# Kernel tuning notes

Hardware: AMD Instinct MI355X
Metric: run time of the kernel (lower is better)

## Reference

```python
import jax, jax.numpy as jnp
import numpy as np

D_MODEL = 1024
N_EXPERTS = 8
TOP_K = 2
D_HIDDEN = 4 * D_MODEL


def setup_inputs() -> dict:
    key = jax.random.key(0)
    ks = jax.random.split(key, 6)
    x = jax.random.normal(ks[0], (4, 2048, D_MODEL), dtype=jnp.float32)
    gate_w = jax.random.normal(ks[1], (N_EXPERTS, D_MODEL), dtype=jnp.float32) * 0.02
    w1 = jax.random.normal(ks[2], (N_EXPERTS, D_MODEL, D_HIDDEN), dtype=jnp.float32) * 0.02
    b1 = jnp.zeros((N_EXPERTS, D_HIDDEN), dtype=jnp.float32)
    w2 = jax.random.normal(ks[3], (N_EXPERTS, D_HIDDEN, D_MODEL), dtype=jnp.float32) * 0.02
    b2 = jnp.zeros((N_EXPERTS, D_MODEL), dtype=jnp.float32)
    return {"x": x, "gate_w": gate_w, "w1": w1, "b1": b1, "w2": w2, "b2": b2}


def reference(x, gate_w, w1, b1, w2, b2):
    B, S, D = x.shape
    xf = x.reshape(-1, D)                               # [T, D]
    logits = xf @ gate_w.T                              # [T, E]
    top_vals, top_idx = jax.lax.top_k(logits, TOP_K)    # [T, K]
    rw = jax.nn.softmax(top_vals.astype(jnp.float32), axis=-1).astype(x.dtype)  # [T, K]
    out = jnp.zeros_like(xf)
    for i in range(N_EXPERTS):
        # combined routing weight for expert i per token (0 if not selected)
        cw = jnp.sum(jnp.where(top_idx == i, rw, jnp.zeros_like(rw)), axis=-1)  # [T]
        h = jax.nn.relu(xf @ w1[i] + b1[i])             # [T, 4D]
        y = h @ w2[i] + b2[i]                           # [T, D]
        out = out + y * cw[:, None]
    return out.reshape(B, S, D)
```

## Files before the change

### kernel.cpp

```cpp
#include <hip/hip_runtime.h>
#include <stdint.h>

#define D_MODEL   1024
#define N_EXPERTS 8
#define D_HIDDEN  4096
#define T_TOKENS  8192
#define N_SLOTS   (T_TOKENS * 2)
#define MAX_TILES 136

typedef __bf16 bf16x8 __attribute__((ext_vector_type(8)));
typedef float  f32x4  __attribute__((ext_vector_type(4)));
typedef unsigned short ushort8 __attribute__((ext_vector_type(8)));

__device__ __forceinline__ unsigned short f2bf(float f) {
    unsigned int u = __float_as_uint(f);
    u += 0x7fffu + ((u >> 16) & 1u);
    return (unsigned short)(u >> 16);
}
__device__ __forceinline__ float bf2f(unsigned short v) {
    return __uint_as_float((unsigned int)v << 16);
}

__device__ __forceinline__ void gl_lds16(const void* g, void* l) {
    __builtin_amdgcn_global_load_lds(
        (const __attribute__((address_space(1))) unsigned int*)g,
        (__attribute__((address_space(3))) unsigned int*)l, 16, 0, 0);
}

__global__ __launch_bounds__(256) void gate_kernel(
    const float* __restrict__ x, const float* __restrict__ gw,
    unsigned short* __restrict__ xb,
    int* __restrict__ route_pack, float* __restrict__ route_w,
    int* __restrict__ cnt)
{
    __shared__ float gws[N_EXPERTS * D_MODEL];
    __shared__ int hist[N_EXPERTS];
    int tid = threadIdx.x;
    for (int i = tid * 4; i < N_EXPERTS * D_MODEL; i += 256 * 4)
        *(float4*)&gws[i] = *(const float4*)&gw[i];
    if (tid < N_EXPERTS) hist[tid] = 0;
    __syncthreads();

    int wave = tid >> 6, lane = tid & 63;
    for (int tt = 0; tt < 4; tt++) {
        int t = blockIdx.x * 16 + wave * 4 + tt;
        const float* xr = x + (size_t)t * D_MODEL;

        float acc[N_EXPERTS];
        for (int e = 0; e < N_EXPERTS; e++) acc[e] = 0.f;
        for (int i = 0; i < 4; i++) {
            float4 xv = *(const float4*)&xr[lane * 4 + i * 256];
            ushort4 o;
            o.x = f2bf(xv.x); o.y = f2bf(xv.y); o.z = f2bf(xv.z); o.w = f2bf(xv.w);
            *(ushort4*)&xb[(size_t)t * D_MODEL + lane * 4 + i * 256] = o;
            for (int e = 0; e < N_EXPERTS; e++) {
                float4 gv = *(const float4*)&gws[e * D_MODEL + lane * 4 + i * 256];
                acc[e] += xv.x * gv.x + xv.y * gv.y + xv.z * gv.z + xv.w * gv.w;
            }
        }
        for (int e = 0; e < N_EXPERTS; e++)
            for (int off = 32; off >= 1; off >>= 1)
                acc[e] += __shfl_xor(acc[e], off, 64);

        if (lane == 0) {
            int e0 = 0; float v0 = acc[0];
            for (int e = 1; e < N_EXPERTS; e++) if (acc[e] > v0) { v0 = acc[e]; e0 = e; }
            int e1 = (e0 == 0) ? 1 : 0; float v1 = acc[e1];
            for (int e = 0; e < N_EXPERTS; e++)
                if (e != e0 && acc[e] > v1) { v1 = acc[e]; e1 = e; }
            float w0 = 1.f / (1.f + __expf(v1 - v0));
            route_pack[t] = e0 | (e1 << 8);
            route_w[2 * t]     = w0;
            route_w[2 * t + 1] = 1.f - w0;
            atomicAdd(&hist[e0], 1);
            atomicAdd(&hist[e1], 1);
        }
    }
    __syncthreads();
    if (tid < N_EXPERTS) atomicAdd(&cnt[tid], hist[tid]);
}

__global__ void offsets_kernel(const int* __restrict__ cnt,
                               int* __restrict__ off, int* __restrict__ cnt2)
{
    if (threadIdx.x == 0) {
        int a = 0;
        for (int e = 0; e < N_EXPERTS; e++) { off[e] = a; a += cnt[e]; cnt2[e] = 0; }
        off[N_EXPERTS] = a;
    }
}

__global__ __launch_bounds__(64) void scatter_kernel(
    const int* __restrict__ route_pack, const int* __restrict__ off,
    int* __restrict__ cnt2, int* __restrict__ tok_id, int* __restrict__ inv)
{
    int lane = threadIdx.x;
    int t = blockIdx.x * 64 + lane;
    int p  = route_pack[t];
    int e0 = p & 0xff, e1 = (p >> 8) & 0xff;

    unsigned long long m0[N_EXPERTS], m1[N_EXPERTS];
    for (int e = 0; e < N_EXPERTS; e++) {
        m0[e] = __ballot(e0 == e);
        m1[e] = __ballot(e1 == e);
    }
    int mybase = 0;
    if (lane < N_EXPERTS)
        mybase = atomicAdd(&cnt2[lane], __popcll(m0[lane]) + __popcll(m1[lane]));

    unsigned long long lt = (1ull << lane) - 1ull;
    int b0 = __shfl(mybase, e0);
    int s0 = off[e0] + b0 + (int)__popcll(m0[e0] & lt);
    int b1 = __shfl(mybase, e1);
    int s1 = off[e1] + b1 + (int)__popcll(m0[e1]) + (int)__popcll(m1[e1] & lt);

    tok_id[s0] = t;
    tok_id[s1] = t;
    inv[2 * t]     = s0;
    inv[2 * t + 1] = s1;
}

template <int R, int C>
__global__ __launch_bounds__(256) void transpose_convert_kernel(
    const float* __restrict__ src, unsigned short* __restrict__ dst)
{
    __shared__ float tile[64 * 68];
    int e = blockIdx.z;
    const float* s = src + (size_t)e * R * C;
    unsigned short* d = dst + (size_t)e * R * C;
    int r0 = blockIdx.y * 64, c0 = blockIdx.x * 64;
    int t = threadIdx.x;
    {
        int r = t >> 4, c4 = (t & 15) * 4;
        for (int p = 0; p < 4; p++, r += 16)
            *(float4*)&tile[r * 68 + c4] = *(const float4*)&s[(size_t)(r0 + r) * C + c0 + c4];
    }
    __syncthreads();
    {
        int c = t >> 2, rblk = (t & 3) * 8;
        for (int q = 0; q < 2; q++) {
            int rr = q * 32 + rblk;
            ushort8 o;
            for (int j = 0; j < 8; j++) o[j] = f2bf(tile[(rr + j) * 68 + c]);
            *(ushort8*)&d[(size_t)(c0 + c) * R + r0 + rr] = o;
        }
    }
}

__global__ __launch_bounds__(256) void gemm1_kernel(
    const unsigned short* __restrict__ xb, const unsigned short* __restrict__ w1t,
    const float* __restrict__ b1, const int* __restrict__ tok_id,
    const int* __restrict__ off, unsigned short* __restrict__ h)
{
    __shared__ unsigned short smem[2 * 128 * 64];
    unsigned short* As = smem;
    unsigned short* Bs = smem + 128 * 64;
    unsigned short* stage = smem;

    int bx = blockIdx.x;
    int e = -1, slot0 = 0, end = 0;
    {
        int acc = 0;
        for (int i = 0; i < N_EXPERTS; i++) {
            int s = off[i], en = off[i + 1];
            int nt = (en - s + 127) >> 7;
            if (e < 0 && bx < acc + nt) { e = i; slot0 = s + (bx - acc) * 128; end = en; }
            acc += nt;
        }
        if (e < 0) return;
    }
    int n0 = blockIdx.y * 128;
    int tid = threadIdx.x, wave = tid >> 6, lane = tid & 63;
    int lr = lane >> 3, lc = lane & 7;

    f32x4 acc[4][4];
    const f32x4 zero = {0.f, 0.f, 0.f, 0.f};
    for (int i = 0; i < 4; i++) for (int j = 0; j < 4; j++) acc[i][j] = zero;

    const unsigned short* gA[4];
    const unsigned short* gB[4];
    unsigned short* lA[4];
    unsigned short* lB[4];
#pragma unroll
    for (int c = 0; c < 4; c++) {
        int arow = wave * 32 + c * 8 + lr;
        int slot = min(slot0 + arow, end - 1);
        gA[c] = xb + (size_t)tok_id[slot] * D_MODEL + lc * 8;
        gB[c] = w1t + ((size_t)e * D_HIDDEN + n0 + arow) * D_MODEL + lc * 8;
        lA[c] = &As[(wave * 32 + c * 8) * 64];
        lB[c] = &Bs[(wave * 32 + c * 8) * 64];
    }

    int wm = wave & 1, wn = wave >> 1;
    int row16 = lane & 15, q8 = (lane >> 4) * 8;
    for (int k0 = 0; k0 < D_MODEL; k0 += 64) {
#pragma unroll
        for (int c = 0; c < 4; c++) {
            gl_lds16(gA[c] + k0, lA[c]);
            gl_lds16(gB[c] + k0, lB[c]);
        }
        __syncthreads();
#pragma unroll
        for (int ks = 0; ks < 2; ks++) {
            bf16x8 af[4], bfr[4];
#pragma unroll
            for (int i = 0; i < 4; i++)
                af[i] = *(const bf16x8*)&As[(wm * 64 + i * 16 + row16) * 64 + ks * 32 + q8];
#pragma unroll
            for (int j = 0; j < 4; j++)
                bfr[j] = *(const bf16x8*)&Bs[(wn * 64 + j * 16 + row16) * 64 + ks * 32 + q8];
#pragma unroll
            for (int i = 0; i < 4; i++)
#pragma unroll
                for (int j = 0; j < 4; j++)
                    acc[i][j] = __builtin_amdgcn_mfma_f32_16x16x32_bf16(af[i], bfr[j], acc[i][j], 0, 0, 0);
        }
        __syncthreads();
    }

    int quad = lane >> 4, col16 = lane & 15;
    for (int p = 0; p < 2; p++) {
        __syncthreads();
        if (wm == p) {
            for (int j = 0; j < 4; j++) {
                int n = n0 + wn * 64 + j * 16 + col16;
                float bias = b1[e * D_HIDDEN + n];
                for (int i = 0; i < 4; i++)
                    for (int r = 0; r < 4; r++) {
                        float v = acc[i][j][r] + bias;
                        v = v > 0.f ? v : 0.f;
                        stage[(i * 16 + quad * 4 + r) * 136 + wn * 64 + j * 16 + col16] = f2bf(v);
                    }
            }
        }
        __syncthreads();
        int row = tid >> 4, coff = (tid & 15) * 8;
        for (int rr = row; rr < 64; rr += 16) {
            int slot = slot0 + p * 64 + rr;
            if (slot < end)
                *(ushort8*)&h[(size_t)slot * D_HIDDEN + n0 + coff] =
                    *(const ushort8*)&stage[rr * 136 + coff];
        }
    }
}

__global__ __launch_bounds__(256) void gemm2_kernel(
    const unsigned short* __restrict__ h, const unsigned short* __restrict__ w2t,
    const float* __restrict__ b2, const int* __restrict__ off,
    unsigned short* __restrict__ y)
{
    __shared__ unsigned short smem[2 * 128 * 64];
    unsigned short* As = smem;
    unsigned short* Bs = smem + 128 * 64;
    unsigned short* stage = smem;

    int bx = blockIdx.x;
    int e = -1, slot0 = 0, end = 0;
    {
        int acc = 0;
        for (int i = 0; i < N_EXPERTS; i++) {
            int s = off[i], en = off[i + 1];
            int nt = (en - s + 127) >> 7;
            if (e < 0 && bx < acc + nt) { e = i; slot0 = s + (bx - acc) * 128; end = en; }
            acc += nt;
        }
        if (e < 0) return;
    }
    int n0 = blockIdx.y * 128;
    int tid = threadIdx.x, wave = tid >> 6, lane = tid & 63;
    int lr = lane >> 3, lc = lane & 7;

    f32x4 acc[4][4];
    const f32x4 zero = {0.f, 0.f, 0.f, 0.f};
    for (int i = 0; i < 4; i++) for (int j = 0; j < 4; j++) acc[i][j] = zero;

    const unsigned short* gA[4];
    const unsigned short* gB[4];
    unsigned short* lA[4];
    unsigned short* lB[4];
#pragma unroll
    for (int c = 0; c < 4; c++) {
        int arow = wave * 32 + c * 8 + lr;
        int slot = min(slot0 + arow, end - 1);
        gA[c] = h + (size_t)slot * D_HIDDEN + lc * 8;
        gB[c] = w2t + ((size_t)e * D_MODEL + n0 + arow) * D_HIDDEN + lc * 8;
        lA[c] = &As[(wave * 32 + c * 8) * 64];
        lB[c] = &Bs[(wave * 32 + c * 8) * 64];
    }

    int wm = wave & 1, wn = wave >> 1;
    int row16 = lane & 15, q8 = (lane >> 4) * 8;
    for (int k0 = 0; k0 < D_HIDDEN; k0 += 64) {
#pragma unroll
        for (int c = 0; c < 4; c++) {
            gl_lds16(gA[c] + k0, lA[c]);
            gl_lds16(gB[c] + k0, lB[c]);
        }
        __syncthreads();
#pragma unroll
        for (int ks = 0; ks < 2; ks++) {
            bf16x8 af[4], bfr[4];
#pragma unroll
            for (int i = 0; i < 4; i++)
                af[i] = *(const bf16x8*)&As[(wm * 64 + i * 16 + row16) * 64 + ks * 32 + q8];
#pragma unroll
            for (int j = 0; j < 4; j++)
                bfr[j] = *(const bf16x8*)&Bs[(wn * 64 + j * 16 + row16) * 64 + ks * 32 + q8];
#pragma unroll
            for (int i = 0; i < 4; i++)
#pragma unroll
                for (int j = 0; j < 4; j++)
                    acc[i][j] = __builtin_amdgcn_mfma_f32_16x16x32_bf16(af[i], bfr[j], acc[i][j], 0, 0, 0);
        }
        __syncthreads();
    }

    int quad = lane >> 4, col16 = lane & 15;
    for (int p = 0; p < 2; p++) {
        __syncthreads();
        if (wm == p) {
            for (int j = 0; j < 4; j++) {
                int n = n0 + wn * 64 + j * 16 + col16;
                float bias = b2[e * D_MODEL + n];
                for (int i = 0; i < 4; i++)
                    for (int r = 0; r < 4; r++) {
                        float v = acc[i][j][r] + bias;
                        stage[(i * 16 + quad * 4 + r) * 136 + wn * 64 + j * 16 + col16] = f2bf(v);
                    }
            }
        }
        __syncthreads();
        int row = tid >> 4, coff = (tid & 15) * 8;
        for (int rr = row; rr < 64; rr += 16) {
            int slot = slot0 + p * 64 + rr;
            if (slot < end)
                *(ushort8*)&y[(size_t)slot * D_MODEL + n0 + coff] =
                    *(const ushort8*)&stage[rr * 136 + coff];
        }
    }
}

__global__ __launch_bounds__(256) void combine_kernel(
    const unsigned short* __restrict__ y, const int* __restrict__ inv,
    const float* __restrict__ rw, float* __restrict__ out)
{
    int wave = threadIdx.x >> 6, lane = threadIdx.x & 63;
    int t = blockIdx.x * 4 + wave;
    int s0 = inv[2 * t], s1 = inv[2 * t + 1];
    float w0 = rw[2 * t], w1 = rw[2 * t + 1];
    const unsigned short* y0 = y + (size_t)s0 * D_MODEL;
    const unsigned short* y1 = y + (size_t)s1 * D_MODEL;
    float* orow = out + (size_t)t * D_MODEL;
    int c = lane * 16;
    for (int hh = 0; hh < 2; hh++) {
        ushort8 a = *(const ushort8*)&y0[c + hh * 8];
        ushort8 b = *(const ushort8*)&y1[c + hh * 8];
        float4 o0, o1;
        o0.x = w0 * bf2f(a[0]) + w1 * bf2f(b[0]);
        o0.y = w0 * bf2f(a[1]) + w1 * bf2f(b[1]);
        o0.z = w0 * bf2f(a[2]) + w1 * bf2f(b[2]);
        o0.w = w0 * bf2f(a[3]) + w1 * bf2f(b[3]);
        o1.x = w0 * bf2f(a[4]) + w1 * bf2f(b[4]);
        o1.y = w0 * bf2f(a[5]) + w1 * bf2f(b[5]);
        o1.z = w0 * bf2f(a[6]) + w1 * bf2f(b[6]);
        o1.w = w0 * bf2f(a[7]) + w1 * bf2f(b[7]);
        *(float4*)&orow[c + hh * 8]     = o0;
        *(float4*)&orow[c + hh * 8 + 4] = o1;
    }
}

extern "C" void kernel_launch(void* const* d_in, const int* in_sizes, int n_in,
                              void* d_out, int out_size, void* d_ws, size_t ws_size,
                              hipStream_t stream)
{
    const float* x      = (const float*)d_in[0];
    const float* gate_w = (const float*)d_in[1];
    const float* w1     = (const float*)d_in[2];
    const float* b1     = (const float*)d_in[3];
    const float* w2     = (const float*)d_in[4];
    const float* b2     = (const float*)d_in[5];
    float* out = (float*)d_out;

    char* ws = (char*)d_ws;
    size_t o = 0;
    auto alloc = [&](size_t bytes) { void* p = ws + o; o += (bytes + 255) & ~(size_t)255; return p; };
    int*   cnt        = (int*)alloc(32);
    int*   cnt2       = (int*)alloc(32);
    int*   off        = (int*)alloc(64);
    int*   route_pack = (int*)alloc((size_t)T_TOKENS * 4);
    float* route_w    = (float*)alloc((size_t)T_TOKENS * 8);
    int*   tok_id     = (int*)alloc((size_t)N_SLOTS * 4);
    int*   inv        = (int*)alloc((size_t)T_TOKENS * 8);
    unsigned short* xb  = (unsigned short*)alloc((size_t)T_TOKENS * D_MODEL * 2);
    unsigned short* w1t = (unsigned short*)alloc((size_t)N_EXPERTS * D_MODEL * D_HIDDEN * 2);
    unsigned short* w2t = (unsigned short*)alloc((size_t)N_EXPERTS * D_MODEL * D_HIDDEN * 2);
    unsigned short* h   = (unsigned short*)alloc((size_t)N_SLOTS * D_HIDDEN * 2);
    unsigned short* y   = w1t;

    hipMemsetAsync(cnt, 0, 32, stream);

    gate_kernel<<<T_TOKENS / 16, 256, 0, stream>>>(x, gate_w, xb, route_pack, route_w, cnt);
    offsets_kernel<<<1, 64, 0, stream>>>(cnt, off, cnt2);
    scatter_kernel<<<T_TOKENS / 64, 64, 0, stream>>>(route_pack, off, cnt2, tok_id, inv);
    transpose_convert_kernel<D_MODEL, D_HIDDEN>
        <<<dim3(D_HIDDEN / 64, D_MODEL / 64, N_EXPERTS), dim3(256), 0, stream>>>(w1, w1t);
    transpose_convert_kernel<D_HIDDEN, D_MODEL>
        <<<dim3(D_MODEL / 64, D_HIDDEN / 64, N_EXPERTS), dim3(256), 0, stream>>>(w2, w2t);
    gemm1_kernel<<<dim3(MAX_TILES, D_HIDDEN / 128), 256, 0, stream>>>(xb, w1t, b1, tok_id, off, h);
    gemm2_kernel<<<dim3(MAX_TILES, D_MODEL / 128), 256, 0, stream>>>(h, w2t, b2, off, y);
    combine_kernel<<<T_TOKENS / 4, 256, 0, stream>>>(y, inv, route_w, out);
}
```

Measured before the change: 902.1 us.

## Double-buffer LDS, XOR-swizzle tiles, and remap blocks across XCDs in expert GEMMs

Both expert GEMM kernels now keep two LDS buffers so the next K-slice's global-to-LDS loads are issued while MFMAs run on the current slice, which drops one barrier per iteration. Columns are XOR-swizzled on load and read to avoid LDS bank conflicts. The 2D grid is flattened to 1D and remapped so consecutive tiles of the same row block land on the same XCD, aiming for better L2 reuse of weights and activations. The cost is double the LDS per block (64KB), which may lower occupancy.

```diff
diff --git a/kernel.cpp b/kernel.cpp
--- a/kernel.cpp
+++ b/kernel.cpp
@@ -152,12 +152,16 @@
     const float* __restrict__ b1, const int* __restrict__ tok_id,
     const int* __restrict__ off, unsigned short* __restrict__ h)
 {
-    __shared__ unsigned short smem[2 * 128 * 64];
-    unsigned short* As = smem;
-    unsigned short* Bs = smem + 128 * 64;
+    constexpr int NT = D_HIDDEN / 128;
+    constexpr int BUF = 128 * 64;
+    __shared__ unsigned short smem[2 * 2 * BUF];
     unsigned short* stage = smem;
 
-    int bx = blockIdx.x;
+    int wg = blockIdx.x;
+    int sz = (wg & 7) * ((MAX_TILES * NT) >> 3) + (wg >> 3);
+    int bx = sz >> 5;
+    int n0 = (sz & (NT - 1)) * 128;
+
     int e = -1, slot0 = 0, end = 0;
     {
         int acc = 0;
@@ -169,9 +173,9 @@
         }
         if (e < 0) return;
     }
-    int n0 = blockIdx.y * 128;
     int tid = threadIdx.x, wave = tid >> 6, lane = tid & 63;
     int lr = lane >> 3, lc = lane & 7;
+    int lcs = lc ^ lr;
 
     f32x4 acc[4][4];
     const f32x4 zero = {0.f, 0.f, 0.f, 0.f};
@@ -179,36 +183,50 @@
 
     const unsigned short* gA[4];
     const unsigned short* gB[4];
-    unsigned short* lA[4];
-    unsigned short* lB[4];
+    int ldsA[4], ldsB[4];
 #pragma unroll
     for (int c = 0; c < 4; c++) {
         int arow = wave * 32 + c * 8 + lr;
         int slot = min(slot0 + arow, end - 1);
-        gA[c] = xb + (size_t)tok_id[slot] * D_MODEL + lc * 8;
-        gB[c] = w1t + ((size_t)e * D_HIDDEN + n0 + arow) * D_MODEL + lc * 8;
-        lA[c] = &As[(wave * 32 + c * 8) * 64];
-        lB[c] = &Bs[(wave * 32 + c * 8) * 64];
+        gA[c] = xb + (size_t)tok_id[slot] * D_MODEL + lcs * 8;
+        gB[c] = w1t + ((size_t)e * D_HIDDEN + n0 + arow) * D_MODEL + lcs * 8;
+        ldsA[c] = (wave * 32 + c * 8) * 64;
+        ldsB[c] = BUF + (wave * 32 + c * 8) * 64;
     }
 
     int wm = wave & 1, wn = wave >> 1;
-    int row16 = lane & 15, q8 = (lane >> 4) * 8;
-    for (int k0 = 0; k0 < D_MODEL; k0 += 64) {
-#pragma unroll
-        for (int c = 0; c < 4; c++) {
-            gl_lds16(gA[c] + k0, lA[c]);
-            gl_lds16(gB[c] + k0, lB[c]);
-        }
-        __syncthreads();
+    int row16 = lane & 15, q4 = lane >> 4;
+    int sx = row16 & 7;
+
+#pragma unroll
+    for (int c = 0; c < 4; c++) {
+        gl_lds16(gA[c], smem + ldsA[c]);
+        gl_lds16(gB[c], smem + ldsB[c]);
+    }
+    __syncthreads();
+
+    int cur = 0;
+    for (int t = 0; t < D_MODEL / 64; t++) {
+        if (t + 1 < D_MODEL / 64) {
+            int k0 = (t + 1) * 64;
+            unsigned short* dst = smem + (cur ^ 1) * 2 * BUF;
+#pragma unroll
+            for (int c = 0; c < 4; c++) {
+                gl_lds16(gA[c] + k0, dst + ldsA[c]);
+                gl_lds16(gB[c] + k0, dst + ldsB[c]);
+            }
+        }
+        const unsigned short* As = smem + cur * 2 * BUF;
+        const unsigned short* Bs = As + BUF;
 #pragma unroll
         for (int ks = 0; ks < 2; ks++) {
             bf16x8 af[4], bfr[4];
 #pragma unroll
             for (int i = 0; i < 4; i++)
-                af[i] = *(const bf16x8*)&As[(wm * 64 + i * 16 + row16) * 64 + ks * 32 + q8];
+                af[i] = *(const bf16x8*)&As[(wm * 64 + i * 16 + row16) * 64 + (((ks * 4 + q4) ^ sx) * 8)];
 #pragma unroll
             for (int j = 0; j < 4; j++)
-                bfr[j] = *(const bf16x8*)&Bs[(wn * 64 + j * 16 + row16) * 64 + ks * 32 + q8];
+                bfr[j] = *(const bf16x8*)&Bs[(wn * 64 + j * 16 + row16) * 64 + (((ks * 4 + q4) ^ sx) * 8)];
 #pragma unroll
             for (int i = 0; i < 4; i++)
 #pragma unroll
@@ -216,6 +234,7 @@
                     acc[i][j] = __builtin_amdgcn_mfma_f32_16x16x32_bf16(af[i], bfr[j], acc[i][j], 0, 0, 0);
         }
         __syncthreads();
+        cur ^= 1;
     }
 
     int quad = lane >> 4, col16 = lane & 15;
@@ -249,12 +268,16 @@
     const float* __restrict__ b2, const int* __restrict__ off,
     unsigned short* __restrict__ y)
 {
-    __shared__ unsigned short smem[2 * 128 * 64];
-    unsigned short* As = smem;
-    unsigned short* Bs = smem + 128 * 64;
+    constexpr int NT = D_MODEL / 128;
+    constexpr int BUF = 128 * 64;
+    __shared__ unsigned short smem[2 * 2 * BUF];
     unsigned short* stage = smem;
 
-    int bx = blockIdx.x;
+    int wg = blockIdx.x;
+    int sz = (wg & 7) * ((MAX_TILES * NT) >> 3) + (wg >> 3);
+    int bx = sz >> 3;
+    int n0 = (sz & (NT - 1)) * 128;
+
     int e = -1, slot0 = 0, end = 0;
     {
         int acc = 0;
@@ -266,9 +289,9 @@
         }
         if (e < 0) return;
     }
-    int n0 = blockIdx.y * 128;
     int tid = threadIdx.x, wave = tid >> 6, lane = tid & 63;
     int lr = lane >> 3, lc = lane & 7;
+    int lcs = lc ^ lr;
 
     f32x4 acc[4][4];
     const f32x4 zero = {0.f, 0.f, 0.f, 0.f};
@@ -276,36 +299,50 @@
 
     const unsigned short* gA[4];
     const unsigned short* gB[4];
-    unsigned short* lA[4];
-    unsigned short* lB[4];
+    int ldsA[4], ldsB[4];
 #pragma unroll
     for (int c = 0; c < 4; c++) {
         int arow = wave * 32 + c * 8 + lr;
         int slot = min(slot0 + arow, end - 1);
-        gA[c] = h + (size_t)slot * D_HIDDEN + lc * 8;
-        gB[c] = w2t + ((size_t)e * D_MODEL + n0 + arow) * D_HIDDEN + lc * 8;
-        lA[c] = &As[(wave * 32 + c * 8) * 64];
-        lB[c] = &Bs[(wave * 32 + c * 8) * 64];
+        gA[c] = h + (size_t)slot * D_HIDDEN + lcs * 8;
+        gB[c] = w2t + ((size_t)e * D_MODEL + n0 + arow) * D_HIDDEN + lcs * 8;
+        ldsA[c] = (wave * 32 + c * 8) * 64;
+        ldsB[c] = BUF + (wave * 32 + c * 8) * 64;
     }
 
     int wm = wave & 1, wn = wave >> 1;
-    int row16 = lane & 15, q8 = (lane >> 4) * 8;
-    for (int k0 = 0; k0 < D_HIDDEN; k0 += 64) {
-#pragma unroll
-        for (int c = 0; c < 4; c++) {
-            gl_lds16(gA[c] + k0, lA[c]);
-            gl_lds16(gB[c] + k0, lB[c]);
-        }
-        __syncthreads();
+    int row16 = lane & 15, q4 = lane >> 4;
+    int sx = row16 & 7;
+
+#pragma unroll
+    for (int c = 0; c < 4; c++) {
+        gl_lds16(gA[c], smem + ldsA[c]);
+        gl_lds16(gB[c], smem + ldsB[c]);
+    }
+    __syncthreads();
+
+    int cur = 0;
+    for (int t = 0; t < D_HIDDEN / 64; t++) {
+        if (t + 1 < D_HIDDEN / 64) {
+            int k0 = (t + 1) * 64;
+            unsigned short* dst = smem + (cur ^ 1) * 2 * BUF;
+#pragma unroll
+            for (int c = 0; c < 4; c++) {
+                gl_lds16(gA[c] + k0, dst + ldsA[c]);
+                gl_lds16(gB[c] + k0, dst + ldsB[c]);
+            }
+        }
+        const unsigned short* As = smem + cur * 2 * BUF;
+        const unsigned short* Bs = As + BUF;
 #pragma unroll
         for (int ks = 0; ks < 2; ks++) {
             bf16x8 af[4], bfr[4];
 #pragma unroll
             for (int i = 0; i < 4; i++)
-                af[i] = *(const bf16x8*)&As[(wm * 64 + i * 16 + row16) * 64 + ks * 32 + q8];
+                af[i] = *(const bf16x8*)&As[(wm * 64 + i * 16 + row16) * 64 + (((ks * 4 + q4) ^ sx) * 8)];
 #pragma unroll
             for (int j = 0; j < 4; j++)
-                bfr[j] = *(const bf16x8*)&Bs[(wn * 64 + j * 16 + row16) * 64 + ks * 32 + q8];
+                bfr[j] = *(const bf16x8*)&Bs[(wn * 64 + j * 16 + row16) * 64 + (((ks * 4 + q4) ^ sx) * 8)];
 #pragma unroll
             for (int i = 0; i < 4; i++)
 #pragma unroll
@@ -313,6 +350,7 @@
                     acc[i][j] = __builtin_amdgcn_mfma_f32_16x16x32_bf16(af[i], bfr[j], acc[i][j], 0, 0, 0);
         }
         __syncthreads();
+        cur ^= 1;
     }
 
     int quad = lane >> 4, col16 = lane & 15;
@@ -406,7 +444,7 @@
         <<<dim3(D_HIDDEN / 64, D_MODEL / 64, N_EXPERTS), dim3(256), 0, stream>>>(w1, w1t);
     transpose_convert_kernel<D_HIDDEN, D_MODEL>
         <<<dim3(D_MODEL / 64, D_HIDDEN / 64, N_EXPERTS), dim3(256), 0, stream>>>(w2, w2t);
-    gemm1_kernel<<<dim3(MAX_TILES, D_HIDDEN / 128), 256, 0, stream>>>(xb, w1t, b1, tok_id, off, h);
-    gemm2_kernel<<<dim3(MAX_TILES, D_MODEL / 128), 256, 0, stream>>>(h, w2t, b2, off, y);
+    gemm1_kernel<<<dim3(MAX_TILES * (D_HIDDEN / 128)), 256, 0, stream>>>(xb, w1t, b1, tok_id, off, h);
+    gemm2_kernel<<<dim3(MAX_TILES * (D_MODEL / 128)), 256, 0, stream>>>(h, w2t, b2, off, y);
     combine_kernel<<<T_TOKENS / 4, 256, 0, stream>>>(y, inv, route_w, out);
 }
```

Result: faster. 773.2 us (-14.3%).

## Rework MoE grouped GEMMs with 256x128 tiles, triple-buffered LDS pipeline, swizzle, XCD remap

Applied to the files above, without the earlier changes.

Both expert GEMMs are merged into one templated kernel that uses 512-thread blocks computing 256x128 tiles, so the weight tiles are read from memory fewer times. Global-to-LDS loads are triple-buffered, with vmcnt waits and raw barriers replacing full __syncthreads, so loads overlap the MFMA work. LDS columns are XOR-swizzled to avoid bank conflicts, and a 1D grid is remapped so that adjacent tiles land on the same XCD for L2 reuse. The costs are more LDS per block (three buffers), higher register pressure, and more padded rows wasted on experts whose token counts are small.

```diff
diff --git a/kernel.cpp b/kernel.cpp
--- a/kernel.cpp
+++ b/kernel.cpp
@@ -6,7 +6,7 @@
 #define D_HIDDEN  4096
 #define T_TOKENS  8192
 #define N_SLOTS   (T_TOKENS * 2)
-#define MAX_TILES 136
+#define MAX_MT    71
 
 typedef __bf16 bf16x8 __attribute__((ext_vector_type(8)));
 typedef float  f32x4  __attribute__((ext_vector_type(4)));
@@ -147,195 +147,144 @@
     }
 }
 
-__global__ __launch_bounds__(256) void gemm1_kernel(
-    const unsigned short* __restrict__ xb, const unsigned short* __restrict__ w1t,
-    const float* __restrict__ b1, const int* __restrict__ tok_id,
-    const int* __restrict__ off, unsigned short* __restrict__ h)
-{
-    __shared__ unsigned short smem[2 * 128 * 64];
-    unsigned short* As = smem;
-    unsigned short* Bs = smem + 128 * 64;
-    unsigned short* stage = smem;
-
-    int bx = blockIdx.x;
+template<int KDIM, int NC, bool RELU, bool USE_TOK>
+__global__ __launch_bounds__(512, 2) void moe_gemm_kernel(
+    const unsigned short* __restrict__ Ag, const unsigned short* __restrict__ Bw,
+    const float* __restrict__ bias, const int* __restrict__ tok_id,
+    const int* __restrict__ off, unsigned short* __restrict__ Cout)
+{
+    constexpr int NT   = KDIM / 64;
+    constexpr int NTN  = NC / 128;
+    constexpr int NWG  = MAX_MT * NTN;
+    constexpr int ASH  = 256 * 64;
+    constexpr int BUFS = (256 + 128) * 64;
+    __shared__ unsigned short smem[3 * BUFS];
+
+    int wg = blockIdx.x;
+    constexpr int qq8 = NWG / 8, rr8 = NWG % 8;
+    int xcd = wg & 7, idx = wg >> 3;
+    int sz = (xcd < rr8 ? xcd * (qq8 + 1) : rr8 * (qq8 + 1) + (xcd - rr8) * qq8) + idx;
+    int bx = sz / NTN;
+    int n0 = (sz % NTN) * 128;
+
     int e = -1, slot0 = 0, end = 0;
     {
         int acc = 0;
         for (int i = 0; i < N_EXPERTS; i++) {
             int s = off[i], en = off[i + 1];
-            int nt = (en - s + 127) >> 7;
-            if (e < 0 && bx < acc + nt) { e = i; slot0 = s + (bx - acc) * 128; end = en; }
+            int nt = (en - s + 255) >> 8;
+            if (e < 0 && bx < acc + nt) { e = i; slot0 = s + (bx - acc) * 256; end = en; }
             acc += nt;
         }
         if (e < 0) return;
     }
-    int n0 = blockIdx.y * 128;
+
     int tid = threadIdx.x, wave = tid >> 6, lane = tid & 63;
+    int wm = wave >> 2, wn = wave & 3;
     int lr = lane >> 3, lc = lane & 7;
-
-    f32x4 acc[4][4];
+    int lcs = lc ^ lr;
+    int row16 = lane & 15, qk = lane >> 4;
+    int sx = row16 & 7;
+
+    f32x4 acc[8][2];
     const f32x4 zero = {0.f, 0.f, 0.f, 0.f};
-    for (int i = 0; i < 4; i++) for (int j = 0; j < 4; j++) acc[i][j] = zero;
+#pragma unroll
+    for (int i = 0; i < 8; i++) { acc[i][0] = zero; acc[i][1] = zero; }
 
     const unsigned short* gA[4];
-    const unsigned short* gB[4];
-    unsigned short* lA[4];
-    unsigned short* lB[4];
+    const unsigned short* gB[2];
+    int ldsA[4], ldsB[2];
 #pragma unroll
     for (int c = 0; c < 4; c++) {
         int arow = wave * 32 + c * 8 + lr;
-        int slot = min(slot0 + arow, end - 1);
-        gA[c] = xb + (size_t)tok_id[slot] * D_MODEL + lc * 8;
-        gB[c] = w1t + ((size_t)e * D_HIDDEN + n0 + arow) * D_MODEL + lc * 8;
-        lA[c] = &As[(wave * 32 + c * 8) * 64];
-        lB[c] = &Bs[(wave * 32 + c * 8) * 64];
-    }
-
-    int wm = wave & 1, wn = wave >> 1;
-    int row16 = lane & 15, q8 = (lane >> 4) * 8;
-    for (int k0 = 0; k0 < D_MODEL; k0 += 64) {
-#pragma unroll
-        for (int c = 0; c < 4; c++) {
-            gl_lds16(gA[c] + k0, lA[c]);
-            gl_lds16(gB[c] + k0, lB[c]);
-        }
-        __syncthreads();
+        int slotc = min(slot0 + arow, end - 1);
+        int grow;
+        if constexpr (USE_TOK) grow = tok_id[slotc]; else grow = slotc;
+        gA[c] = Ag + (size_t)grow * KDIM + lcs * 8;
+        ldsA[c] = (wave * 32 + c * 8) * 64;
+    }
+#pragma unroll
+    for (int c = 0; c < 2; c++) {
+        int brow = wave * 16 + c * 8 + lr;
+        gB[c] = Bw + ((size_t)e * NC + n0 + brow) * KDIM + lcs * 8;
+        ldsB[c] = ASH + (wave * 16 + c * 8) * 64;
+    }
+
+    auto stage = [&](int b, int kt) {
+        unsigned short* base = smem + b * BUFS;
+#pragma unroll
+        for (int c = 0; c < 4; c++) gl_lds16(gA[c] + kt * 64, base + ldsA[c]);
+#pragma unroll
+        for (int c = 0; c < 2; c++) gl_lds16(gB[c] + kt * 64, base + ldsB[c]);
+    };
+
+    stage(0, 0);
+    stage(1, 1);
+    asm volatile("s_waitcnt vmcnt(6)" ::: "memory");
+    __builtin_amdgcn_s_barrier();
+
+    int cur = 0, nb = 2;
+    for (int t = 0; t < NT; t++) {
+        stage(nb, min(t + 2, NT - 1));
+        const unsigned short* Ab = smem + cur * BUFS;
+        const unsigned short* Bb = Ab + ASH;
+        __builtin_amdgcn_s_setprio(1);
 #pragma unroll
         for (int ks = 0; ks < 2; ks++) {
-            bf16x8 af[4], bfr[4];
-#pragma unroll
-            for (int i = 0; i < 4; i++)
-                af[i] = *(const bf16x8*)&As[(wm * 64 + i * 16 + row16) * 64 + ks * 32 + q8];
-#pragma unroll
-            for (int j = 0; j < 4; j++)
-                bfr[j] = *(const bf16x8*)&Bs[(wn * 64 + j * 16 + row16) * 64 + ks * 32 + q8];
-#pragma unroll
-            for (int i = 0; i < 4; i++)
-#pragma unroll
-                for (int j = 0; j < 4; j++)
-                    acc[i][j] = __builtin_amdgcn_mfma_f32_16x16x32_bf16(af[i], bfr[j], acc[i][j], 0, 0, 0);
-        }
-        __syncthreads();
-    }
-
-    int quad = lane >> 4, col16 = lane & 15;
+            bf16x8 af[8], bq[2];
+#pragma unroll
+            for (int i = 0; i < 8; i++) {
+                int rr = wm * 128 + i * 16 + row16;
+                af[i] = *(const bf16x8*)&Ab[rr * 64 + (((ks * 4 + qk) ^ sx) * 8)];
+            }
+#pragma unroll
+            for (int j = 0; j < 2; j++) {
+                int br = wn * 32 + j * 16 + row16;
+                bq[j] = *(const bf16x8*)&Bb[br * 64 + (((ks * 4 + qk) ^ sx) * 8)];
+            }
+#pragma unroll
+            for (int i = 0; i < 8; i++)
+#pragma unroll
+                for (int j = 0; j < 2; j++)
+                    acc[i][j] = __builtin_amdgcn_mfma_f32_16x16x32_bf16(af[i], bq[j], acc[i][j], 0, 0, 0);
+        }
+        __builtin_amdgcn_s_setprio(0);
+        asm volatile("s_waitcnt vmcnt(6)" ::: "memory");
+        __builtin_amdgcn_s_barrier();
+        cur = (cur + 1) == 3 ? 0 : cur + 1;
+        nb  = (nb + 1)  == 3 ? 0 : nb + 1;
+    }
+
+    asm volatile("s_waitcnt vmcnt(0) lgkmcnt(0)" ::: "memory");
+    __syncthreads();
+    unsigned short* stg = smem;
+    int quad = lane >> 4, c16 = lane & 15;
     for (int p = 0; p < 2; p++) {
-        __syncthreads();
+        if (p) __syncthreads();
         if (wm == p) {
-            for (int j = 0; j < 4; j++) {
-                int n = n0 + wn * 64 + j * 16 + col16;
-                float bias = b1[e * D_HIDDEN + n];
-                for (int i = 0; i < 4; i++)
+#pragma unroll
+            for (int j = 0; j < 2; j++) {
+                int n = n0 + wn * 32 + j * 16 + c16;
+                float bv = bias[e * NC + n];
+#pragma unroll
+                for (int i = 0; i < 8; i++)
+#pragma unroll
                     for (int r = 0; r < 4; r++) {
-                        float v = acc[i][j][r] + bias;
-                        v = v > 0.f ? v : 0.f;
-                        stage[(i * 16 + quad * 4 + r) * 136 + wn * 64 + j * 16 + col16] = f2bf(v);
+                        float v = acc[i][j][r] + bv;
+                        if (RELU) v = v > 0.f ? v : 0.f;
+                        stg[(i * 16 + quad * 4 + r) * 136 + wn * 32 + j * 16 + c16] = f2bf(v);
                     }
             }
         }
         __syncthreads();
-        int row = tid >> 4, coff = (tid & 15) * 8;
-        for (int rr = row; rr < 64; rr += 16) {
-            int slot = slot0 + p * 64 + rr;
+        int srow = tid >> 4, chunk = (tid & 15) * 8;
+#pragma unroll
+        for (int s8 = 0; s8 < 4; s8++) {
+            int rr = srow + s8 * 32;
+            int slot = slot0 + p * 128 + rr;
             if (slot < end)
-                *(ushort8*)&h[(size_t)slot * D_HIDDEN + n0 + coff] =
-                    *(const ushort8*)&stage[rr * 136 + coff];
-        }
-    }
-}
-
-__global__ __launch_bounds__(256) void gemm2_kernel(
-    const unsigned short* __restrict__ h, const unsigned short* __restrict__ w2t,
-    const float* __restrict__ b2, const int* __restrict__ off,
-    unsigned short* __restrict__ y)
-{
-    __shared__ unsigned short smem[2 * 128 * 64];
-    unsigned short* As = smem;
-    unsigned short* Bs = smem + 128 * 64;
-    unsigned short* stage = smem;
-
-    int bx = blockIdx.x;
-    int e = -1, slot0 = 0, end = 0;
-    {
-        int acc = 0;
-        for (int i = 0; i < N_EXPERTS; i++) {
-            int s = off[i], en = off[i + 1];
-            int nt = (en - s + 127) >> 7;
-            if (e < 0 && bx < acc + nt) { e = i; slot0 = s + (bx - acc) * 128; end = en; }
-            acc += nt;
-        }
-        if (e < 0) return;
-    }
-    int n0 = blockIdx.y * 128;
-    int tid = threadIdx.x, wave = tid >> 6, lane = tid & 63;
-    int lr = lane >> 3, lc = lane & 7;
-
-    f32x4 acc[4][4];
-    const f32x4 zero = {0.f, 0.f, 0.f, 0.f};
-    for (int i = 0; i < 4; i++) for (int j = 0; j < 4; j++) acc[i][j] = zero;
-
-    const unsigned short* gA[4];
-    const unsigned short* gB[4];
-    unsigned short* lA[4];
-    unsigned short* lB[4];
-#pragma unroll
-    for (int c = 0; c < 4; c++) {
-        int arow = wave * 32 + c * 8 + lr;
-        int slot = min(slot0 + arow, end - 1);
-        gA[c] = h + (size_t)slot * D_HIDDEN + lc * 8;
-        gB[c] = w2t + ((size_t)e * D_MODEL + n0 + arow) * D_HIDDEN + lc * 8;
-        lA[c] = &As[(wave * 32 + c * 8) * 64];
-        lB[c] = &Bs[(wave * 32 + c * 8) * 64];
-    }
-
-    int wm = wave & 1, wn = wave >> 1;
-    int row16 = lane & 15, q8 = (lane >> 4) * 8;
-    for (int k0 = 0; k0 < D_HIDDEN; k0 += 64) {
-#pragma unroll
-        for (int c = 0; c < 4; c++) {
-            gl_lds16(gA[c] + k0, lA[c]);
-            gl_lds16(gB[c] + k0, lB[c]);
-        }
-        __syncthreads();
-#pragma unroll
-        for (int ks = 0; ks < 2; ks++) {
-            bf16x8 af[4], bfr[4];
-#pragma unroll
-            for (int i = 0; i < 4; i++)
-                af[i] = *(const bf16x8*)&As[(wm * 64 + i * 16 + row16) * 64 + ks * 32 + q8];
-#pragma unroll
-            for (int j = 0; j < 4; j++)
-                bfr[j] = *(const bf16x8*)&Bs[(wn * 64 + j * 16 + row16) * 64 + ks * 32 + q8];
-#pragma unroll
-            for (int i = 0; i < 4; i++)
-#pragma unroll
-                for (int j = 0; j < 4; j++)
-                    acc[i][j] = __builtin_amdgcn_mfma_f32_16x16x32_bf16(af[i], bfr[j], acc[i][j], 0, 0, 0);
-        }
-        __syncthreads();
-    }
-
-    int quad = lane >> 4, col16 = lane & 15;
-    for (int p = 0; p < 2; p++) {
-        __syncthreads();
-        if (wm == p) {
-            for (int j = 0; j < 4; j++) {
-                int n = n0 + wn * 64 + j * 16 + col16;
-                float bias = b2[e * D_MODEL + n];
-                for (int i = 0; i < 4; i++)
-                    for (int r = 0; r < 4; r++) {
-                        float v = acc[i][j][r] + bias;
-                        stage[(i * 16 + quad * 4 + r) * 136 + wn * 64 + j * 16 + col16] = f2bf(v);
-                    }
-            }
-        }
-        __syncthreads();
-        int row = tid >> 4, coff = (tid & 15) * 8;
-        for (int rr = row; rr < 64; rr += 16) {
-            int slot = slot0 + p * 64 + rr;
-            if (slot < end)
-                *(ushort8*)&y[(size_t)slot * D_MODEL + n0 + coff] =
-                    *(const ushort8*)&stage[rr * 136 + coff];
+                *(ushort8*)&Cout[(size_t)slot * NC + n0 + chunk] =
+                    *(const ushort8*)&stg[rr * 136 + chunk];
         }
     }
 }
@@ -406,7 +355,9 @@
         <<<dim3(D_HIDDEN / 64, D_MODEL / 64, N_EXPERTS), dim3(256), 0, stream>>>(w1, w1t);
     transpose_convert_kernel<D_HIDDEN, D_MODEL>
         <<<dim3(D_MODEL / 64, D_HIDDEN / 64, N_EXPERTS), dim3(256), 0, stream>>>(w2, w2t);
-    gemm1_kernel<<<dim3(MAX_TILES, D_HIDDEN / 128), 256, 0, stream>>>(xb, w1t, b1, tok_id, off, h);
-    gemm2_kernel<<<dim3(MAX_TILES, D_MODEL / 128), 256, 0, stream>>>(h, w2t, b2, off, y);
+    moe_gemm_kernel<D_MODEL, D_HIDDEN, true, true>
+        <<<dim3(MAX_MT * (D_HIDDEN / 128)), dim3(512), 0, stream>>>(xb, w1t, b1, tok_id, off, h);
+    moe_gemm_kernel<D_HIDDEN, D_MODEL, false, false>
+        <<<dim3(MAX_MT * (D_MODEL / 128)), dim3(512), 0, stream>>>(h, w2t, b2, tok_id, off, y);
     combine_kernel<<<T_TOKENS / 4, 256, 0, stream>>>(y, inv, route_w, out);
 }
```

Result: faster. 744.6 us (-17.5%).
